# Kernel tuning notes

Measured on AMD Instinct MI355X. Metric: run time of the kernel, lower is better.

Reference implementation:

```python
import jax, jax.numpy as jnp
import numpy as np

# SGCN (AsynSpiGCN) internals are not in the source; reconstructed as a standard
# LIF spiking-GCN: per time step, spikes propagate along edges weighted by
# edge_attr (gather src -> scatter-add dst), membrane potential decays with
# decay_alpha, neurons fire above threshold unless refractory, reset to v_r.
V_REST = 0.0
V_R = 0.0
SPEED = 1.0
THRESH = 0.5
REFRAC = 2.0
DECAY = 0.8
T_STEPS = 8
BETA = 0.5

N_NODES = 50000
N_EDGES = 800000
IN_DIM = 256
HID_DIM = 128


def setup_inputs() -> dict:
    key = jax.random.key(0)
    k1, k2, k3, k4, k5 = jax.random.split(key, 5)
    x = jax.random.normal(k1, (N_NODES, IN_DIM), dtype=jnp.float32)
    spike_node = jax.random.randint(k2, (N_NODES,), 0, 2, dtype=jnp.int32)
    edge_index = jax.random.randint(k3, (2, N_EDGES), 0, N_NODES, dtype=jnp.int32)
    node_indices = jnp.arange(N_NODES, dtype=jnp.int32)
    edge_attr = jax.random.uniform(k4, (N_EDGES,), dtype=jnp.float32)
    W = jax.random.normal(k5, (IN_DIM, HID_DIM), dtype=jnp.float32) * 0.05
    b = jnp.zeros((HID_DIM,), dtype=jnp.float32)
    return {"x": x, "spike_node": spike_node, "edge_index": edge_index,
            "node_indices": node_indices, "edge_attr": edge_attr, "W": W, "b": b}


def reference(x, spike_node, edge_index, node_indices, edge_attr, W, b):
    N = x.shape[0]
    # Linear projection + per-feature min-max standardization over nodes (dim 0)
    h = x @ W + b
    mn = h.min(axis=0, keepdims=True)
    mx = h.max(axis=0, keepdims=True)
    h = (h - mn) / (mx - mn + 1e-6)

    src, dst = edge_index[0], edge_index[1]
    v0 = jnp.full_like(h, V_REST)            # membrane potential [N, H]
    ref0 = jnp.zeros_like(h)                 # refractory counters [N, H]
    s0 = jnp.broadcast_to(spike_node.astype(h.dtype)[:, None], h.shape)

    def step(carry, _):
        v, ref, s = carry
        msg = s[src] * edge_attr[:, None]                      # [E, H] gather
        agg = jax.ops.segment_sum(msg, dst, num_segments=N)    # [N, H] scatter-add
        v = DECAY * v + SPEED * h + agg
        can_fire = ref <= 0
        spk = ((v >= THRESH) & can_fire).astype(h.dtype)
        v = jnp.where(spk > 0, V_R, v)
        ref = jnp.where(spk > 0, REFRAC, jnp.maximum(ref - 1.0, 0.0))
        return (v, ref, spk), spk

    (vT, _, _), spike_matrix = jax.lax.scan(step, (v0, ref0, s0), None, length=T_STEPS)
    fusion_tensor = h + BETA * vT
    return fusion_tensor, spike_matrix
```

## Files before the change

kernel.cpp:

```cpp
#include <hip/hip_runtime.h>
#include <cstdint>

#define N_NODES 50000
#define N_EDGES 800000
#define IN_DIM  256
#define HID     128
#define T_STEPS 8

static __device__ __forceinline__ unsigned int enc_f(float f) {
    unsigned int u = __float_as_uint(f);
    return (u & 0x80000000u) ? ~u : (u | 0x80000000u);
}
static __device__ __forceinline__ float dec_f(unsigned int u) {
    unsigned int b = (u & 0x80000000u) ? (u ^ 0x80000000u) : ~u;
    return __uint_as_float(b);
}

__global__ void k_count(const int* __restrict__ dst, int* __restrict__ counts) {
    int e = blockIdx.x * blockDim.x + threadIdx.x;
    if (e < N_EDGES) atomicAdd(&counts[dst[e]], 1);
}

__global__ void k_scan1(const int* __restrict__ counts, int* __restrict__ row_tmp,
                        int* __restrict__ blocksum) {
    __shared__ int sh[256];
    int t = threadIdx.x, i = blockIdx.x * 256 + t;
    int c = (i < N_NODES) ? counts[i] : 0;
    sh[t] = c; __syncthreads();
    for (int off = 1; off < 256; off <<= 1) {
        int val = (t >= off) ? sh[t - off] : 0;
        __syncthreads();
        sh[t] += val;
        __syncthreads();
    }
    if (i < N_NODES) row_tmp[i] = sh[t] - c;
    if (t == 255) blocksum[blockIdx.x] = sh[255];
}

__global__ void k_scan2(const int* __restrict__ blocksum, int* __restrict__ blockoff,
                        int nb, int* __restrict__ row_ptr) {
    if (threadIdx.x == 0) {
        int acc = 0;
        for (int b = 0; b < nb; ++b) { blockoff[b] = acc; acc += blocksum[b]; }
        row_ptr[N_NODES] = acc;
    }
}

__global__ void k_scan3(const int* __restrict__ row_tmp, const int* __restrict__ blockoff,
                        int* __restrict__ row_ptr) {
    int i = blockIdx.x * blockDim.x + threadIdx.x;
    if (i < N_NODES) row_ptr[i] = row_tmp[i] + blockoff[i >> 8];
}

__global__ void k_fill(const int* __restrict__ dst, const int* __restrict__ src,
                       const float* __restrict__ attr,
                       const int* __restrict__ row_ptr, int* __restrict__ cursor,
                       int* __restrict__ eid, int2* __restrict__ edata) {
    int e = blockIdx.x * blockDim.x + threadIdx.x;
    if (e >= N_EDGES) return;
    int d = dst[e];
    int p = row_ptr[d] + atomicAdd(&cursor[d], 1);
    eid[p]   = e;
    edata[p] = make_int2(src[e], __float_as_int(attr[e]));
}

__global__ __launch_bounds__(256) void k_bsort(const int* __restrict__ row_ptr,
                                               int* __restrict__ eid,
                                               int2* __restrict__ edata) {
    int node = blockIdx.x * 4 + (threadIdx.x >> 6);
    int l = threadIdx.x & 63;
    int beg = row_ptr[node], end = row_ptr[node + 1], cnt = end - beg;
    if (cnt <= 1) return;
    if (cnt <= 64) {
        int key = 0x7FFFFFFF, sv = 0, av = 0;
        if (l < cnt) { key = eid[beg + l]; int2 d = edata[beg + l]; sv = d.x; av = d.y; }
        #pragma unroll
        for (int k = 2; k <= 64; k <<= 1) {
            for (int j = k >> 1; j > 0; j >>= 1) {
                int pk = __shfl_xor(key, j);
                int ps = __shfl_xor(sv, j);
                int pa = __shfl_xor(av, j);
                bool lower = (l & j) == 0;
                bool asc   = (l & k) == 0;
                bool take_min = (lower == asc);
                bool take = take_min ? (pk < key) : (pk > key);
                if (take) { key = pk; sv = ps; av = pa; }
            }
        }
        if (l < cnt) { eid[beg + l] = key; edata[beg + l] = make_int2(sv, av); }
    } else if (l == 0) {
        for (int i = beg + 1; i < end; ++i) {
            int ke = eid[i]; int2 kd = edata[i];
            int m = i - 1;
            while (m >= beg && eid[m] > ke) {
                eid[m+1] = eid[m]; edata[m+1] = edata[m]; --m;
            }
            eid[m+1] = ke; edata[m+1] = kd;
        }
    }
}

__global__ __launch_bounds__(256) void k_gemm(const float* __restrict__ x,
                                              const float* __restrict__ W,
                                              const float* __restrict__ b,
                                              float* __restrict__ h,
                                              unsigned int* __restrict__ mn_e,
                                              unsigned int* __restrict__ mx_e) {
    __shared__ float Ws[32 * 128];
    __shared__ float xs[64 * 36];
    __shared__ float red_mn[8 * 128];
    __shared__ float red_mx[8 * 128];
    const int tid = threadIdx.x;
    const int n0 = blockIdx.x * 64;
    const int jt = tid & 31, nt = tid >> 5;
    const int j0 = jt * 4;

    float acc[8][4];
    #pragma unroll
    for (int a = 0; a < 8; ++a)
        #pragma unroll
        for (int c = 0; c < 4; ++c) acc[a][c] = 0.0f;

    const int ldn = tid >> 2;
    const int kq  = (tid & 3) * 8;
    const int xrow = (n0 + ldn < N_NODES) ? (n0 + ldn) : (N_NODES - 1);
    const float* xg = x + (size_t)xrow * IN_DIM;

    for (int kc = 0; kc < IN_DIM; kc += 32) {
        __syncthreads();
        float4 xa = *(const float4*)(xg + kc + kq);
        float4 xb = *(const float4*)(xg + kc + kq + 4);
        *(float4*)&xs[ldn * 36 + kq]     = xa;
        *(float4*)&xs[ldn * 36 + kq + 4] = xb;
        #pragma unroll
        for (int p = 0; p < 4; ++p) {
            int r = nt + p * 8;
            *(float4*)&Ws[r * 128 + j0] =
                *(const float4*)(W + (size_t)(kc + r) * HID + j0);
        }
        __syncthreads();
        const float* xbase = &xs[nt * 8 * 36];
        #pragma unroll 4
        for (int k = 0; k < 32; ++k) {
            float4 wf = *(const float4*)&Ws[k * 128 + j0];
            #pragma unroll
            for (int ni = 0; ni < 8; ++ni) {
                float xv = xbase[ni * 36 + k];
                acc[ni][0] = __fmaf_rn(xv, wf.x, acc[ni][0]);
                acc[ni][1] = __fmaf_rn(xv, wf.y, acc[ni][1]);
                acc[ni][2] = __fmaf_rn(xv, wf.z, acc[ni][2]);
                acc[ni][3] = __fmaf_rn(xv, wf.w, acc[ni][3]);
            }
        }
    }

    float4 bv = *(const float4*)(b + j0);
    float lmn[4], lmx[4];
    #pragma unroll
    for (int c = 0; c < 4; ++c) { lmn[c] = INFINITY; lmx[c] = -INFINITY; }
    #pragma unroll
    for (int ni = 0; ni < 8; ++ni) {
        acc[ni][0] = __fadd_rn(acc[ni][0], bv.x);
        acc[ni][1] = __fadd_rn(acc[ni][1], bv.y);
        acc[ni][2] = __fadd_rn(acc[ni][2], bv.z);
        acc[ni][3] = __fadd_rn(acc[ni][3], bv.w);
        #pragma unroll
        for (int c = 0; c < 4; ++c) {
            lmn[c] = fminf(lmn[c], acc[ni][c]);
            lmx[c] = fmaxf(lmx[c], acc[ni][c]);
        }
    }
    #pragma unroll
    for (int c = 0; c < 4; ++c) {
        red_mn[nt * 128 + j0 + c] = lmn[c];
        red_mx[nt * 128 + j0 + c] = lmx[c];
    }
    __syncthreads();
    if (tid < 128) {
        float mnv = red_mn[tid], mxv = red_mx[tid];
        #pragma unroll
        for (int r = 1; r < 8; ++r) {
            mnv = fminf(mnv, red_mn[r * 128 + tid]);
            mxv = fmaxf(mxv, red_mx[r * 128 + tid]);
        }
        atomicMin(&mn_e[tid], enc_f(mnv));
        atomicMax(&mx_e[tid], enc_f(mxv));
    }
    #pragma unroll
    for (int ni = 0; ni < 8; ++ni) {
        int n = n0 + nt * 8 + ni;
        if (n < N_NODES)
            *(float4*)&h[(size_t)n * HID + j0] =
                make_float4(acc[ni][0], acc[ni][1], acc[ni][2], acc[ni][3]);
    }
}

__global__ void k_init_bits(const int* __restrict__ spike_node, uint32_t* __restrict__ sb) {
    int n = blockIdx.x * blockDim.x + threadIdx.x;
    if (n >= N_NODES) return;
    uint32_t f = spike_node[n] ? 0xFFFFFFFFu : 0u;
    sb[(size_t)n * 4 + 0] = f;
    sb[(size_t)n * 4 + 1] = f;
    sb[(size_t)n * 4 + 2] = f;
    sb[(size_t)n * 4 + 3] = f;
}

static __device__ __forceinline__ void gbar2(int* bar, int nblk) {
    __syncthreads();
    if (threadIdx.x == 0) {
        __threadfence();
        const int l   = blockIdx.x & 7;
        const int lsz = (nblk - l + 7) >> 3;
        int* lc = bar + l * 64;
        int* lg = bar + 512 + l * 64;
        int* rc = bar + 1024;
        int* rg = bar + 1088;
        int gl = __hip_atomic_load(lg, __ATOMIC_RELAXED, __HIP_MEMORY_SCOPE_AGENT);
        int a  = __hip_atomic_fetch_add(lc, 1, __ATOMIC_ACQ_REL, __HIP_MEMORY_SCOPE_AGENT);
        if (a == lsz - 1) {
            __hip_atomic_store(lc, 0, __ATOMIC_RELAXED, __HIP_MEMORY_SCOPE_AGENT);
            int gr = __hip_atomic_load(rg, __ATOMIC_RELAXED, __HIP_MEMORY_SCOPE_AGENT);
            int r  = __hip_atomic_fetch_add(rc, 1, __ATOMIC_ACQ_REL, __HIP_MEMORY_SCOPE_AGENT);
            if (r == 7) {
                __hip_atomic_store(rc, 0, __ATOMIC_RELAXED, __HIP_MEMORY_SCOPE_AGENT);
                __hip_atomic_fetch_add(rg, 1, __ATOMIC_ACQ_REL, __HIP_MEMORY_SCOPE_AGENT);
            } else {
                while (__hip_atomic_load(rg, __ATOMIC_RELAXED,
                                         __HIP_MEMORY_SCOPE_AGENT) == gr)
                    __builtin_amdgcn_s_sleep(4);
            }
            __hip_atomic_fetch_add(lg, 1, __ATOMIC_ACQ_REL, __HIP_MEMORY_SCOPE_AGENT);
        } else {
            while (__hip_atomic_load(lg, __ATOMIC_RELAXED,
                                     __HIP_MEMORY_SCOPE_AGENT) == gl)
                __builtin_amdgcn_s_sleep(8);
        }
        __threadfence();
    }
    __syncthreads();
}

template<int TNPB, int TNSLOT, int TECAP, int TPACK, int TMINW>
__global__ __launch_bounds__(256, TMINW) void k_lif_t(
    const int* __restrict__ row_ptr,
    const int2* __restrict__ edata,
    uint32_t* __restrict__ sbA,
    uint32_t* __restrict__ sbB,
    const float* __restrict__ h_raw,
    const unsigned int* __restrict__ mn_e,
    const unsigned int* __restrict__ mx_e,
    float* __restrict__ out,
    int* __restrict__ bar,
    int nblk)
{
    __shared__ int      lrp[TNPB + 1];
    __shared__ int      ed_src_l[TECAP];
    __shared__ float    ed_attr_l[TECAP];
    __shared__ uint32_t ed_wds[TPACK ? 1 : TECAP * 4];
    __shared__ uint2    ed_pk[TPACK ? TECAP * 4 : 1];
    __shared__ uint32_t sbw[TNPB][4];

    const int tid = threadIdx.x;
    const int g   = tid >> 5;
    const int ln  = tid & 31;
    const int n0  = blockIdx.x * TNPB;
    const int ncnt = min(TNPB, N_NODES - n0);
    const int w = ln >> 3, shb = (ln & 7) * 4;
    const size_t NH = (size_t)N_NODES * HID;

    if (tid <= ncnt) lrp[tid] = row_ptr[n0 + tid];
    __syncthreads();
    const int ebase = lrp[0];
    const int etot  = lrp[ncnt] - ebase;
    const bool inlds = (etot <= TECAP);
    if (inlds) {
        for (int i = tid; i < etot; i += 256) {
            int2 d = edata[ebase + i];
            ed_src_l[i]  = d.x;
            ed_attr_l[i] = __int_as_float(d.y);
        }
    }

    uint4 mnu = *(const uint4*)&mn_e[ln * 4];
    uint4 mxu = *(const uint4*)&mx_e[ln * 4];
    float mn0 = dec_f(mnu.x), mn1 = dec_f(mnu.y), mn2 = dec_f(mnu.z), mn3 = dec_f(mnu.w);
    float dd0 = __fadd_rn(__fsub_rn(dec_f(mxu.x), mn0), 1e-6f);
    float dd1 = __fadd_rn(__fsub_rn(dec_f(mxu.y), mn1), 1e-6f);
    float dd2 = __fadd_rn(__fsub_rn(dec_f(mxu.z), mn2), 1e-6f);
    float dd3 = __fadd_rn(__fsub_rn(dec_f(mxu.w), mn3), 1e-6f);

    float4 hs[TNSLOT], vs[TNSLOT];
    uint32_t rcs[TNSLOT];
    #pragma unroll
    for (int s = 0; s < TNSLOT; ++s) {
        hs[s] = make_float4(0.f, 0.f, 0.f, 0.f);
        vs[s] = make_float4(0.f, 0.f, 0.f, 0.f);
        rcs[s] = 0u;
        int m = s * 8 + g;
        if (m < ncnt) {
            size_t idx = (size_t)(n0 + m) * HID + ln * 4;
            float4 t = *(const float4*)&h_raw[idx];
            t.x = __fdiv_rn(__fsub_rn(t.x, mn0), dd0);
            t.y = __fdiv_rn(__fsub_rn(t.y, mn1), dd1);
            t.z = __fdiv_rn(__fsub_rn(t.z, mn2), dd2);
            t.w = __fdiv_rn(__fsub_rn(t.w, mn3), dd3);
            hs[s] = t;
        }
    }
    for (int i = tid; i < ncnt * 4; i += 256) ((uint32_t*)sbw)[i] = 0u;
    __syncthreads();

    for (int t = 0; t < T_STEPS; ++t) {
        const uint32_t* cur = (t & 1) ? sbB : sbA;
        uint32_t*       nxt = (t & 1) ? sbA : sbB;
        if (t > 0) gbar2(bar, nblk);

        if (inlds) {
            for (int i = tid; i < etot; i += 256) {
                uint4 wv = *(const uint4*)&cur[(size_t)ed_src_l[i] * 4];
                if (TPACK) {
                    uint32_t ab = __float_as_uint(ed_attr_l[i]);
                    ed_pk[i * 4 + 0] = make_uint2(ab, wv.x);
                    ed_pk[i * 4 + 1] = make_uint2(ab, wv.y);
                    ed_pk[i * 4 + 2] = make_uint2(ab, wv.z);
                    ed_pk[i * 4 + 3] = make_uint2(ab, wv.w);
                } else {
                    *(uint4*)&ed_wds[i * 4] = wv;
                }
            }
        }
        __syncthreads();

        #pragma unroll
        for (int s = 0; s < TNSLOT; ++s) {
            int m = s * 8 + g;
            if (m < ncnt) {
                float ag0 = 0.f, ag1 = 0.f, ag2 = 0.f, ag3 = 0.f;
                if (inlds) {
                    int lb = lrp[m] - ebase, le = lrp[m + 1] - ebase;
                    for (int i = lb; i < le; ++i) {
                        uint32_t u; float a;
                        if (TPACK) {
                            uint2 p = ed_pk[i * 4 + w];
                            a = __uint_as_float(p.x);
                            u = p.y;
                        } else {
                            u = ed_wds[i * 4 + w];
                            a = ed_attr_l[i];
                        }
                        uint32_t bits = (u >> shb) & 0xFu;
                        ag0 = __fadd_rn(ag0, (bits & 1u) ? a : 0.f);
                        ag1 = __fadd_rn(ag1, (bits & 2u) ? a : 0.f);
                        ag2 = __fadd_rn(ag2, (bits & 4u) ? a : 0.f);
                        ag3 = __fadd_rn(ag3, (bits & 8u) ? a : 0.f);
                    }
                } else {
                    int lb = lrp[m], le = lrp[m + 1];
                    for (int i = lb; i < le; ++i) {
                        int2 d = edata[i];
                        uint32_t u = cur[(size_t)d.x * 4 + w];
                        float a = __int_as_float(d.y);
                        uint32_t bits = (u >> shb) & 0xFu;
                        ag0 = __fadd_rn(ag0, (bits & 1u) ? a : 0.f);
                        ag1 = __fadd_rn(ag1, (bits & 2u) ? a : 0.f);
                        ag2 = __fadd_rn(ag2, (bits & 4u) ? a : 0.f);
                        ag3 = __fadd_rn(ag3, (bits & 8u) ? a : 0.f);
                    }
                }

                float hv[4] = {hs[s].x, hs[s].y, hs[s].z, hs[s].w};
                float vv[4] = {vs[s].x, vs[s].y, vs[s].z, vs[s].w};
                float ag[4] = {ag0, ag1, ag2, ag3};
                float vf[4], sf[4];
                uint32_t rcu = rcs[s], rcn = 0u, nib = 0u;
                #pragma unroll
                for (int q = 0; q < 4; ++q) {
                    float vn = __fadd_rn(__fadd_rn(__fmul_rn(0.8f, vv[q]), hv[q]), ag[q]);
                    uint32_t rc = (rcu >> (8 * q)) & 0xFFu;
                    bool spk = (vn >= 0.5f) && (rc == 0u);
                    vf[q] = spk ? 0.0f : vn;
                    sf[q] = spk ? 1.0f : 0.0f;
                    uint32_t rnew = spk ? 2u : (rc > 0u ? rc - 1u : 0u);
                    rcn |= rnew << (8 * q);
                    nib |= (spk ? 1u : 0u) << q;
                }
                vs[s] = make_float4(vf[0], vf[1], vf[2], vf[3]);
                rcs[s] = rcn;
                size_t idx = (size_t)(n0 + m) * HID + ln * 4;
                *(float4*)&out[NH + (size_t)t * NH + idx] =
                    make_float4(sf[0], sf[1], sf[2], sf[3]);
                if (t == T_STEPS - 1) {
                    *(float4*)&out[idx] = make_float4(
                        __fadd_rn(hv[0], __fmul_rn(0.5f, vf[0])),
                        __fadd_rn(hv[1], __fmul_rn(0.5f, vf[1])),
                        __fadd_rn(hv[2], __fmul_rn(0.5f, vf[2])),
                        __fadd_rn(hv[3], __fmul_rn(0.5f, vf[3])));
                }
                atomicOr(&sbw[m][w], nib << shb);
            }
        }
        __syncthreads();
        for (int i = tid; i < ncnt * 4; i += 256) {
            nxt[(size_t)n0 * 4 + i] = ((uint32_t*)sbw)[i];
            ((uint32_t*)sbw)[i] = 0u;
        }
    }
}

__global__ __launch_bounds__(128) void k_step(const int* __restrict__ row_ptr,
                                              const int2* __restrict__ edata,
                                              const uint32_t* __restrict__ sb_cur,
                                              uint32_t* __restrict__ sb_nxt,
                                              float* __restrict__ h,
                                              float* __restrict__ v,
                                              unsigned char* __restrict__ refc,
                                              const unsigned int* __restrict__ mn_e,
                                              const unsigned int* __restrict__ mx_e,
                                              float* __restrict__ out_spk,
                                              float* __restrict__ out_fus,
                                              int t0, int is_last) {
    __shared__ float    attr_l[4][128];
    __shared__ uint32_t words_l[4][128][4];
    __shared__ uint32_t sbw[16];
    __shared__ int      rp[5];

    const int tid = threadIdx.x;
    const int ns = tid >> 5, ln = tid & 31;
    const int nb = blockIdx.x * 4;
    const int n  = nb + ns;

    if (tid < 16) sbw[tid] = 0;
    if (tid < 5)  rp[tid] = row_ptr[nb + tid];
    __syncthreads();

    const int beg = rp[ns], cnt = rp[ns + 1] - beg;
    int cmax = 0;
    #pragma unroll
    for (int q = 0; q < 4; ++q) cmax = max(cmax, rp[q + 1] - rp[q]);
    const int nchunk = (cmax + 127) >> 7;

    float agg0 = 0.f, agg1 = 0.f, agg2 = 0.f, agg3 = 0.f;
    const int w = ln >> 3, shb = (ln & 7) * 4;

    for (int ch = 0; ch < nchunk; ++ch) {
        int base = ch << 7;
        __syncthreads();
        #pragma unroll
        for (int rep = 0; rep < 4; ++rep) {
            int i = base + rep * 32 + ln;
            if (i < cnt) {
                int2 d = edata[beg + i];
                attr_l[ns][rep * 32 + ln] = __int_as_float(d.y);
                *(uint4*)&words_l[ns][rep * 32 + ln][0] =
                    *(const uint4*)&sb_cur[(size_t)d.x * 4];
            }
        }
        __syncthreads();
        int lim = min(128, cnt - base);
        for (int i = 0; i < lim; ++i) {
            uint32_t u = words_l[ns][i][w];
            float a = attr_l[ns][i];
            uint32_t bits = (u >> shb) & 0xFu;
            agg0 = __fadd_rn(agg0, (bits & 1u) ? a : 0.0f);
            agg1 = __fadd_rn(agg1, (bits & 2u) ? a : 0.0f);
            agg2 = __fadd_rn(agg2, (bits & 4u) ? a : 0.0f);
            agg3 = __fadd_rn(agg3, (bits & 8u) ? a : 0.0f);
        }
    }

    const size_t idx = (size_t)n * HID + ln * 4;
    float4 h4 = *(const float4*)&h[idx];
    if (t0) {
        const int jb = ln * 4;
        float hq[4] = {h4.x, h4.y, h4.z, h4.w};
        #pragma unroll
        for (int q = 0; q < 4; ++q) {
            float mn = dec_f(mn_e[jb + q]);
            float mx = dec_f(mx_e[jb + q]);
            float d2 = __fadd_rn(__fsub_rn(mx, mn), 1e-6f);
            hq[q] = __fdiv_rn(__fsub_rn(hq[q], mn), d2);
        }
        h4 = make_float4(hq[0], hq[1], hq[2], hq[3]);
        *(float4*)&h[idx] = h4;
    }
    float4 v4;
    unsigned int rcu;
    if (t0) { v4 = make_float4(0.f, 0.f, 0.f, 0.f); rcu = 0u; }
    else    { v4 = *(const float4*)&v[idx]; rcu = *(const unsigned int*)&refc[idx]; }

    float hv[4]  = {h4.x, h4.y, h4.z, h4.w};
    float vv[4]  = {v4.x, v4.y, v4.z, v4.w};
    float ag[4]  = {agg0, agg1, agg2, agg3};
    float vf[4], sf[4];
    unsigned int rcn = 0u, nib = 0u;
    #pragma unroll
    for (int q = 0; q < 4; ++q) {
        float vn = __fadd_rn(__fadd_rn(__fmul_rn(0.8f, vv[q]), hv[q]), ag[q]);
        unsigned int rc = (rcu >> (8 * q)) & 0xFFu;
        bool spk = (vn >= 0.5f) && (rc == 0u);
        vf[q] = spk ? 0.0f : vn;
        sf[q] = spk ? 1.0f : 0.0f;
        unsigned int rnew = spk ? 2u : (rc > 0u ? rc - 1u : 0u);
        rcn |= rnew << (8 * q);
        nib |= (spk ? 1u : 0u) << q;
    }
    *(float4*)&v[idx] = make_float4(vf[0], vf[1], vf[2], vf[3]);
    *(unsigned int*)&refc[idx] = rcn;
    *(float4*)&out_spk[idx] = make_float4(sf[0], sf[1], sf[2], sf[3]);
    if (is_last) {
        *(float4*)&out_fus[idx] = make_float4(
            __fadd_rn(hv[0], __fmul_rn(0.5f, vf[0])),
            __fadd_rn(hv[1], __fmul_rn(0.5f, vf[1])),
            __fadd_rn(hv[2], __fmul_rn(0.5f, vf[2])),
            __fadd_rn(hv[3], __fmul_rn(0.5f, vf[3])));
    }
    atomicOr(&sbw[ns * 4 + w], nib << shb);
    __syncthreads();
    if (tid < 16)
        sb_nxt[(size_t)(nb + (tid >> 2)) * 4 + (tid & 3)] = sbw[tid];
}

extern "C" void kernel_launch(void* const* d_in, const int* in_sizes, int n_in,
                              void* d_out, int out_size, void* d_ws, size_t ws_size,
                              hipStream_t stream) {
    const float* x          = (const float*)d_in[0];
    const int*   spike_node = (const int*)  d_in[1];
    const int*   edge_index = (const int*)  d_in[2];
    const float* edge_attr  = (const float*)d_in[4];
    const float* W          = (const float*)d_in[5];
    const float* b          = (const float*)d_in[6];
    float* out = (float*)d_out;

    const int* src = edge_index;
    const int* dst = edge_index + N_EDGES;

    char* wsp = (char*)d_ws;
    auto alloc = [&](size_t bytes) {
        char* p = wsp;
        wsp += (bytes + 255) & ~(size_t)255;
        return p;
    };
    float*         h        = (float*)        alloc((size_t)N_NODES * HID * 4);
    float*         v        = (float*)        alloc((size_t)N_NODES * HID * 4);
    unsigned char* refc     = (unsigned char*)alloc((size_t)N_NODES * HID);
    uint32_t*      sbA      = (uint32_t*)     alloc((size_t)N_NODES * 16);
    uint32_t*      sbB      = (uint32_t*)     alloc((size_t)N_NODES * 16);
    int*           counts   = (int*)          alloc((size_t)N_NODES * 4);
    int*           cursor   = (int*)          alloc((size_t)N_NODES * 4);
    int*           row_tmp  = (int*)          alloc((size_t)N_NODES * 4);
    int*           row_ptr  = (int*)          alloc((size_t)(N_NODES + 1) * 4);
    int*           blocksum = (int*)          alloc(256 * 4);
    int*           blockoff = (int*)          alloc(256 * 4);
    int*           eid      = (int*)          alloc((size_t)N_EDGES * 4);
    int2*          edata    = (int2*)         alloc((size_t)N_EDGES * 8);
    unsigned int*  mn_e     = (unsigned int*) alloc(HID * 4);
    unsigned int*  mx_e     = (unsigned int*) alloc(HID * 4);
    int*           barv     = (int*)          alloc(8192);

    hipMemsetAsync(counts, 0x00, (size_t)N_NODES * 4, stream);
    hipMemsetAsync(cursor, 0x00, (size_t)N_NODES * 4, stream);
    hipMemsetAsync(mn_e,   0xFF, HID * 4, stream);
    hipMemsetAsync(mx_e,   0x00, HID * 4, stream);
    hipMemsetAsync(barv,   0x00, 8192, stream);

    const int NB = (N_NODES + 255) / 256;
    const int EB = (N_EDGES + 255) / 256;

    k_count<<<EB, 256, 0, stream>>>(dst, counts);
    k_scan1<<<NB, 256, 0, stream>>>(counts, row_tmp, blocksum);
    k_scan2<<<1, 64, 0, stream>>>(blocksum, blockoff, NB, row_ptr);
    k_scan3<<<NB, 256, 0, stream>>>(row_tmp, blockoff, row_ptr);
    k_fill<<<EB, 256, 0, stream>>>(dst, src, edge_attr, row_ptr, cursor, eid, edata);
    k_bsort<<<N_NODES / 4, 256, 0, stream>>>(row_ptr, eid, edata);

    k_gemm<<<(N_NODES + 63) / 64, 256, 0, stream>>>(x, W, b, h, mn_e, mx_e);
    k_init_bits<<<NB, 256, 0, stream>>>(spike_node, sbA);

    const size_t NH = (size_t)N_NODES * HID;

    auto kC = k_lif_t<33, 5, 768, 0, 6>;
    auto kD = k_lif_t<40, 5, 896, 0, 5>;
    auto kA = k_lif_t<66, 9, 1536, 0, 3>;
    auto kB = k_lif_t<98, 13, 1920, 1, 2>;
    int occC = 0, occD = 0, occA = 0, occB = 0;
    hipOccupancyMaxActiveBlocksPerMultiprocessor(&occC, kC, 256, 0);
    hipOccupancyMaxActiveBlocksPerMultiprocessor(&occD, kD, 256, 0);
    hipOccupancyMaxActiveBlocksPerMultiprocessor(&occA, kA, 256, 0);
    hipOccupancyMaxActiveBlocksPerMultiprocessor(&occB, kB, 256, 0);

    if (occC >= 6) {
        const int grid = (N_NODES + 32) / 33;
        kC<<<grid, 256, 0, stream>>>(row_ptr, edata, sbA, sbB, h, mn_e, mx_e,
                                     out, barv, grid);
    } else if (occD >= 5) {
        const int grid = (N_NODES + 39) / 40;
        kD<<<grid, 256, 0, stream>>>(row_ptr, edata, sbA, sbB, h, mn_e, mx_e,
                                     out, barv, grid);
    } else if (occA >= 3) {
        const int grid = (N_NODES + 65) / 66;
        kA<<<grid, 256, 0, stream>>>(row_ptr, edata, sbA, sbB, h, mn_e, mx_e,
                                     out, barv, grid);
    } else if (occB >= 2) {
        const int grid = (N_NODES + 97) / 98;
        kB<<<grid, 256, 0, stream>>>(row_ptr, edata, sbA, sbB, h, mn_e, mx_e,
                                     out, barv, grid);
    } else {
        for (int t = 0; t < T_STEPS; ++t) {
            uint32_t* cur = (t & 1) ? sbB : sbA;
            uint32_t* nxt = (t & 1) ? sbA : sbB;
            k_step<<<N_NODES / 4, 128, 0, stream>>>(row_ptr, edata, cur, nxt,
                                                    h, v, refc, mn_e, mx_e,
                                                    out + NH + (size_t)t * NH,
                                                    out, (t == 0) ? 1 : 0,
                                                    (t == T_STEPS - 1) ? 1 : 0);
        }
    }
}
```

Before: 620.7 us.

## Replace hierarchical grid barrier with flag barrier and prefer larger blocks

Swaps the two-level atomic-counter grid barrier for a per-block flag barrier in which block 0 polls all flags and releases a go flag. Spike-bit reads and writes become relaxed agent-scope atomics so cross-block visibility no longer relies on threadfences. The launcher now prefers the 66-node-per-block persistent config, halving the grid and the number of barrier participants. Relaxed ordering without fences risks stale spike data, and larger blocks may reduce parallelism.

```diff
diff --git a/kernel.cpp b/kernel.cpp
--- a/kernel.cpp
+++ b/kernel.cpp
@@ -205,39 +205,33 @@
     sb[(size_t)n * 4 + 3] = f;
 }
 
-static __device__ __forceinline__ void gbar2(int* bar, int nblk) {
+static __device__ __forceinline__ void fbar(int* bar, int nblk, int t) {
+    int* flags = bar;
+    int* go    = bar + 1900;
     __syncthreads();
-    if (threadIdx.x == 0) {
-        __threadfence();
-        const int l   = blockIdx.x & 7;
-        const int lsz = (nblk - l + 7) >> 3;
-        int* lc = bar + l * 64;
-        int* lg = bar + 512 + l * 64;
-        int* rc = bar + 1024;
-        int* rg = bar + 1088;
-        int gl = __hip_atomic_load(lg, __ATOMIC_RELAXED, __HIP_MEMORY_SCOPE_AGENT);
-        int a  = __hip_atomic_fetch_add(lc, 1, __ATOMIC_ACQ_REL, __HIP_MEMORY_SCOPE_AGENT);
-        if (a == lsz - 1) {
-            __hip_atomic_store(lc, 0, __ATOMIC_RELAXED, __HIP_MEMORY_SCOPE_AGENT);
-            int gr = __hip_atomic_load(rg, __ATOMIC_RELAXED, __HIP_MEMORY_SCOPE_AGENT);
-            int r  = __hip_atomic_fetch_add(rc, 1, __ATOMIC_ACQ_REL, __HIP_MEMORY_SCOPE_AGENT);
-            if (r == 7) {
-                __hip_atomic_store(rc, 0, __ATOMIC_RELAXED, __HIP_MEMORY_SCOPE_AGENT);
-                __hip_atomic_fetch_add(rg, 1, __ATOMIC_ACQ_REL, __HIP_MEMORY_SCOPE_AGENT);
-            } else {
-                while (__hip_atomic_load(rg, __ATOMIC_RELAXED,
-                                         __HIP_MEMORY_SCOPE_AGENT) == gr)
-                    __builtin_amdgcn_s_sleep(4);
-            }
-            __hip_atomic_fetch_add(lg, 1, __ATOMIC_ACQ_REL, __HIP_MEMORY_SCOPE_AGENT);
-        } else {
-            while (__hip_atomic_load(lg, __ATOMIC_RELAXED,
-                                     __HIP_MEMORY_SCOPE_AGENT) == gl)
-                __builtin_amdgcn_s_sleep(8);
-        }
-        __threadfence();
-    }
-    __syncthreads();
+    if (blockIdx.x == 0) {
+        if (threadIdx.x == 0)
+            __hip_atomic_store(&flags[0], t, __ATOMIC_RELAXED, __HIP_MEMORY_SCOPE_AGENT);
+        for (;;) {
+            int ok = 1;
+            for (int i = (int)threadIdx.x; i < nblk; i += 256)
+                ok &= (__hip_atomic_load(&flags[i], __ATOMIC_RELAXED,
+                                         __HIP_MEMORY_SCOPE_AGENT) >= t);
+            if (__syncthreads_and(ok)) break;
+            __builtin_amdgcn_s_sleep(1);
+        }
+        if (threadIdx.x == 0)
+            __hip_atomic_store(go, t, __ATOMIC_RELAXED, __HIP_MEMORY_SCOPE_AGENT);
+    } else {
+        if (threadIdx.x == 0) {
+            __hip_atomic_store(&flags[blockIdx.x], t, __ATOMIC_RELAXED,
+                               __HIP_MEMORY_SCOPE_AGENT);
+            while (__hip_atomic_load(go, __ATOMIC_RELAXED,
+                                     __HIP_MEMORY_SCOPE_AGENT) < t)
+                __builtin_amdgcn_s_sleep(4);
+        }
+        __syncthreads();
+    }
 }
 
 template<int TNPB, int TNSLOT, int TECAP, int TPACK, int TMINW>
@@ -313,11 +307,19 @@
     for (int t = 0; t < T_STEPS; ++t) {
         const uint32_t* cur = (t & 1) ? sbB : sbA;
         uint32_t*       nxt = (t & 1) ? sbA : sbB;
-        if (t > 0) gbar2(bar, nblk);
+        if (t > 0) fbar(bar, nblk, t);
 
         if (inlds) {
             for (int i = tid; i < etot; i += 256) {
-                uint4 wv = *(const uint4*)&cur[(size_t)ed_src_l[i] * 4];
+                unsigned long long* sp =
+                    (unsigned long long*)&cur[(size_t)ed_src_l[i] * 4];
+                unsigned long long lo = __hip_atomic_load(
+                    sp, __ATOMIC_RELAXED, __HIP_MEMORY_SCOPE_AGENT);
+                unsigned long long hi = __hip_atomic_load(
+                    sp + 1, __ATOMIC_RELAXED, __HIP_MEMORY_SCOPE_AGENT);
+                uint4 wv;
+                wv.x = (uint32_t)lo; wv.y = (uint32_t)(lo >> 32);
+                wv.z = (uint32_t)hi; wv.w = (uint32_t)(hi >> 32);
                 if (TPACK) {
                     uint32_t ab = __float_as_uint(ed_attr_l[i]);
                     ed_pk[i * 4 + 0] = make_uint2(ab, wv.x);
@@ -358,7 +360,9 @@
                     int lb = lrp[m], le = lrp[m + 1];
                     for (int i = lb; i < le; ++i) {
                         int2 d = edata[i];
-                        uint32_t u = cur[(size_t)d.x * 4 + w];
+                        uint32_t u = __hip_atomic_load(
+                            (uint32_t*)&cur[(size_t)d.x * 4 + w],
+                            __ATOMIC_RELAXED, __HIP_MEMORY_SCOPE_AGENT);
                         float a = __int_as_float(d.y);
                         uint32_t bits = (u >> shb) & 0xFu;
                         ag0 = __fadd_rn(ag0, (bits & 1u) ? a : 0.f);
@@ -401,7 +405,8 @@
         }
         __syncthreads();
         for (int i = tid; i < ncnt * 4; i += 256) {
-            nxt[(size_t)n0 * 4 + i] = ((uint32_t*)sbw)[i];
+            __hip_atomic_store(&nxt[(size_t)n0 * 4 + i], ((uint32_t*)sbw)[i],
+                               __ATOMIC_RELAXED, __HIP_MEMORY_SCOPE_AGENT);
             ((uint32_t*)sbw)[i] = 0u;
         }
     }
@@ -578,27 +583,27 @@
 
     const size_t NH = (size_t)N_NODES * HID;
 
+    auto kA = k_lif_t<66, 9, 1536, 0, 3>;
     auto kC = k_lif_t<33, 5, 768, 0, 6>;
     auto kD = k_lif_t<40, 5, 896, 0, 5>;
-    auto kA = k_lif_t<66, 9, 1536, 0, 3>;
     auto kB = k_lif_t<98, 13, 1920, 1, 2>;
-    int occC = 0, occD = 0, occA = 0, occB = 0;
+    int occA = 0, occC = 0, occD = 0, occB = 0;
+    hipOccupancyMaxActiveBlocksPerMultiprocessor(&occA, kA, 256, 0);
     hipOccupancyMaxActiveBlocksPerMultiprocessor(&occC, kC, 256, 0);
     hipOccupancyMaxActiveBlocksPerMultiprocessor(&occD, kD, 256, 0);
-    hipOccupancyMaxActiveBlocksPerMultiprocessor(&occA, kA, 256, 0);
     hipOccupancyMaxActiveBlocksPerMultiprocessor(&occB, kB, 256, 0);
 
-    if (occC >= 6) {
+    if (occA >= 3) {
+        const int grid = (N_NODES + 65) / 66;
+        kA<<<grid, 256, 0, stream>>>(row_ptr, edata, sbA, sbB, h, mn_e, mx_e,
+                                     out, barv, grid);
+    } else if (occC >= 6) {
         const int grid = (N_NODES + 32) / 33;
         kC<<<grid, 256, 0, stream>>>(row_ptr, edata, sbA, sbB, h, mn_e, mx_e,
                                      out, barv, grid);
     } else if (occD >= 5) {
         const int grid = (N_NODES + 39) / 40;
         kD<<<grid, 256, 0, stream>>>(row_ptr, edata, sbA, sbB, h, mn_e, mx_e,
-                                     out, barv, grid);
-    } else if (occA >= 3) {
-        const int grid = (N_NODES + 65) / 66;
-        kA<<<grid, 256, 0, stream>>>(row_ptr, edata, sbA, sbB, h, mn_e, mx_e,
                                      out, barv, grid);
     } else if (occB >= 2) {
         const int grid = (N_NODES + 97) / 98;
```

Result: no change. 625.4 us (+0.7%).
